# Kernel tuning notes

Hardware: AMD Instinct MI355X
Metric: run time of the kernel (lower is better)

Reference implementation:

```python
import jax, jax.numpy as jnp
import numpy as np
from jax import lax

EPS = 1e-12  # F.normalize eps

def setup_inputs() -> dict:
    key = jax.random.key(0)
    k1, k2, k3, k4 = jax.random.split(key, 4)
    b, c, h, w = 4, 64, 256, 256
    x = jax.random.normal(k1, (b, c, h, w), dtype=jnp.float32)
    w_in = jax.random.normal(k2, (4 * c, c), dtype=jnp.float32) * 0.05   # 1x1 conv dim->4*dim
    w_dw = jax.random.normal(k3, (2 * c, 1, 3, 3), dtype=jnp.float32) * 0.05  # depthwise 3x3, groups=2*dim
    w_out = jax.random.normal(k4, (c, c), dtype=jnp.float32) * 0.05      # 1x1 conv dim->dim
    temperature = jnp.ones((1, 1), dtype=jnp.float32)
    return {"x": x, "w_in": w_in, "w_dw": w_dw, "w_out": w_out, "temperature": temperature}


def reference(x, w_in, w_dw, w_out, temperature):
    b, c, h, w = x.shape
    # project_in: 1x1 conv dim -> 4*dim, then chunk into x1 (2c), x2 (2c)
    t = jnp.einsum('oc,bchw->bohw', w_in, x)
    x1, x2 = t[:, :2 * c], t[:, 2 * c:]
    # depthwise 3x3 conv (groups = 2c), padding=1
    dw = lax.conv_general_dilated(
        x1, w_dw, window_strides=(1, 1), padding='SAME',
        feature_group_count=2 * c,
        dimension_numbers=('NCHW', 'OIHW', 'NCHW'))
    qv = dw * x2  # [b, 2c, h, w]
    q = qv[:, :c].reshape(b, c, h * w)
    v = qv[:, c:].reshape(b, c, h * w)
    # L2-normalize along HW (F.normalize with eps)
    qn = q / jnp.maximum(jnp.linalg.norm(q, axis=-1, keepdims=True), EPS)
    kn = v / jnp.maximum(jnp.linalg.norm(v, axis=-1, keepdims=True), EPS)
    # channel-wise attention: [b, c, c]
    attn = jax.nn.softmax(jnp.einsum('bcn,bdn->bcd', qn, kn) * temperature, axis=-1)
    out = jnp.einsum('bcd,bdn->bcn', attn, v).reshape(b, c, h, w)
    # project_out: 1x1 conv dim -> dim
    return jnp.einsum('oc,bchw->bohw', w_out, out)
```

## Files before the change

kernel.cpp:

```cpp
#include <hip/hip_runtime.h>

#define EPSF 1e-12f
#define NT1 512

typedef __attribute__((ext_vector_type(8))) short short8;
typedef __attribute__((ext_vector_type(4))) float f32x4;
typedef __attribute__((ext_vector_type(4))) unsigned int uint4v;
typedef __attribute__((ext_vector_type(2))) unsigned int uint2v;

__device__ __forceinline__ unsigned f2bf(float f) {
    unsigned u = __float_as_uint(f);
    return (u + 0x7FFFu + ((u >> 16) & 1u)) >> 16;
}
__device__ __forceinline__ float bf2f(unsigned h) { return __uint_as_float(h << 16); }
__device__ __forceinline__ short8 asbf(uint4v u) { return __builtin_bit_cast(short8, u); }


__global__ __launch_bounds__(256, 2)
void kQ_half(const float* __restrict__ x, const float* __restrict__ w_in,
             const float* __restrict__ w_dw, unsigned short* __restrict__ qh,
             unsigned* __restrict__ vpk, float* __restrict__ sqq,
             float* __restrict__ sqv)
{
    __shared__ unsigned short t1s[64 * 360];
    __shared__ unsigned short t2s[64 * 264];

    const int tid = threadIdx.x;
    const int wv = tid >> 6, lane = tid & 63;
    const int l15 = lane & 15, l4 = lane >> 4;

    const int blk = blockIdx.x;
    const int half = blk & 1;
    const int tile = (blk >> 1) & 255;
    const int b = blk >> 9;
    const int y0 = (tile >> 3) << 3;
    const int x0t = (tile & 7) << 5;

    uint4v A1h[2], A1l[2], A2h[2], A2l[2];
    #pragma unroll
    for (int kh = 0; kh < 2; ++kh) {
        const float* wp1 = w_in + (half * 64 + wv * 16 + l15) * 64 + kh * 32 + l4 * 8;
        const float* wp2 = wp1 + 128 * 64;
        uint4v h1, l1, h2, l2;
        #pragma unroll
        for (int j = 0; j < 4; ++j) {
            float f0 = wp1[2*j], f1 = wp1[2*j+1];
            unsigned u0 = f2bf(f0), u1 = f2bf(f1);
            h1[j] = (u1 << 16) | u0;
            l1[j] = (f2bf(f1 - bf2f(u1)) << 16) | f2bf(f0 - bf2f(u0));
            float g0 = wp2[2*j], g1 = wp2[2*j+1];
            unsigned v0 = f2bf(g0), v1 = f2bf(g1);
            h2[j] = (v1 << 16) | v0;
            l2[j] = (f2bf(g1 - bf2f(v1)) << 16) | f2bf(g0 - bf2f(v0));
        }
        A1h[kh] = h1; A1l[kh] = l1;
        A2h[kh] = h2; A2l[kh] = l2;
    }

    const float* xb = x + ((size_t)b << 22);

    #pragma unroll 2
    for (int ht = 0; ht < 22; ++ht) {
        const int p = ht * 16 + l15;
        const unsigned row = (unsigned)p / 34u;
        const int col = p - (int)row * 34;
        const int gy = y0 - 1 + (int)row;
        const int gx = x0t - 1 + col;
        const bool inb = (p < 340) && ((unsigned)gy < 256u) && ((unsigned)gx < 256u);

        float xv0[8], xv1[8];
        #pragma unroll
        for (int j = 0; j < 8; ++j) { xv0[j] = 0.f; xv1[j] = 0.f; }
        if (inb) {
            const float* bp = xb + (size_t)(gy * 256 + gx);
            #pragma unroll
            for (int j = 0; j < 8; ++j) {
                xv0[j] = bp[(size_t)(l4 * 8 + j) << 16];
                xv1[j] = bp[(size_t)(32 + l4 * 8 + j) << 16];
            }
        }
        uint4v bh0, bl0, bh1, bl1;
        #pragma unroll
        for (int j = 0; j < 4; ++j) {
            unsigned h0 = f2bf(xv0[2*j]), h1 = f2bf(xv0[2*j+1]);
            bh0[j] = (h1 << 16) | h0;
            bl0[j] = (f2bf(xv0[2*j+1] - bf2f(h1)) << 16) | f2bf(xv0[2*j] - bf2f(h0));
            unsigned g0 = f2bf(xv1[2*j]), g1 = f2bf(xv1[2*j+1]);
            bh1[j] = (g1 << 16) | g0;
            bl1[j] = (f2bf(xv1[2*j+1] - bf2f(g1)) << 16) | f2bf(xv1[2*j] - bf2f(g0));
        }
        const short8 Bh0 = asbf(bh0), Bh1 = asbf(bh1);
        const short8 Bl0 = asbf(bl0), Bl1 = asbf(bl1);

        f32x4 a1 = {0.f, 0.f, 0.f, 0.f};
        a1 = __builtin_amdgcn_mfma_f32_16x16x32_bf16(asbf(A1h[0]), Bh0, a1, 0,0,0);
        a1 = __builtin_amdgcn_mfma_f32_16x16x32_bf16(asbf(A1h[1]), Bh1, a1, 0,0,0);
        a1 = __builtin_amdgcn_mfma_f32_16x16x32_bf16(asbf(A1h[0]), Bl0, a1, 0,0,0);
        a1 = __builtin_amdgcn_mfma_f32_16x16x32_bf16(asbf(A1h[1]), Bl1, a1, 0,0,0);
        a1 = __builtin_amdgcn_mfma_f32_16x16x32_bf16(asbf(A1l[0]), Bh0, a1, 0,0,0);
        a1 = __builtin_amdgcn_mfma_f32_16x16x32_bf16(asbf(A1l[1]), Bh1, a1, 0,0,0);

        f32x4 a2 = {0.f, 0.f, 0.f, 0.f};
        a2 = __builtin_amdgcn_mfma_f32_16x16x32_bf16(asbf(A2h[0]), Bh0, a2, 0,0,0);
        a2 = __builtin_amdgcn_mfma_f32_16x16x32_bf16(asbf(A2h[1]), Bh1, a2, 0,0,0);
        a2 = __builtin_amdgcn_mfma_f32_16x16x32_bf16(asbf(A2h[0]), Bl0, a2, 0,0,0);
        a2 = __builtin_amdgcn_mfma_f32_16x16x32_bf16(asbf(A2h[1]), Bl1, a2, 0,0,0);
        a2 = __builtin_amdgcn_mfma_f32_16x16x32_bf16(asbf(A2l[0]), Bh0, a2, 0,0,0);
        a2 = __builtin_amdgcn_mfma_f32_16x16x32_bf16(asbf(A2l[1]), Bh1, a2, 0,0,0);

        if (p < 340) {
            const int chb = wv * 16 + l4 * 4;
            #pragma unroll
            for (int r = 0; r < 4; ++r)
                t1s[(chb + r) * 360 + (int)row * 36 + col] = (unsigned short)f2bf(a1[r]);
        }
        if (row >= 1u && row <= 8u && col >= 1 && col <= 32) {
            const int cpx = ((int)row - 1) * 32 + (col - 1);
            const int chb = wv * 16 + l4 * 4;
            #pragma unroll
            for (int r = 0; r < 4; ++r)
                t2s[(chb + r) * 264 + cpx] = (unsigned short)f2bf(a2[r]);
        }
    }

    for (int it = 0; it < 8; ++it) {
        const int ch = wv * 16 + it * 2 + (lane >> 5);
        const int strip = lane & 31;
        const int row = strip >> 2, xs0 = (strip & 3) << 3;
        const float* wd = w_dw + (half * 64 + ch) * 9;
        const float w0 = wd[0], w1 = wd[1], w2 = wd[2];
        const float w3 = wd[3], w4 = wd[4], w5 = wd[5];
        const float w6 = wd[6], w7 = wd[7], w8 = wd[8];

        float win[3][10];
        #pragma unroll
        for (int r3 = 0; r3 < 3; ++r3) {
            const unsigned short* tp = &t1s[ch * 360 + (row + r3) * 36 + xs0];
            const uint2v ua = *(const uint2v*)tp;
            const uint2v ub = *(const uint2v*)(tp + 4);
            const unsigned uc = *(const unsigned*)(tp + 8);
            win[r3][0] = bf2f(ua[0] & 0xFFFFu); win[r3][1] = bf2f(ua[0] >> 16);
            win[r3][2] = bf2f(ua[1] & 0xFFFFu); win[r3][3] = bf2f(ua[1] >> 16);
            win[r3][4] = bf2f(ub[0] & 0xFFFFu); win[r3][5] = bf2f(ub[0] >> 16);
            win[r3][6] = bf2f(ub[1] & 0xFFFFu); win[r3][7] = bf2f(ub[1] >> 16);
            win[r3][8] = bf2f(uc & 0xFFFFu);    win[r3][9] = bf2f(uc >> 16);
        }
        const uint4v gv = *(const uint4v*)&t2s[ch * 264 + row * 32 + xs0];

        float q8[8];
        float sq = 0.f;
        #pragma unroll
        for (int k = 0; k < 8; ++k) {
            const float dwv = w0*win[0][k] + w1*win[0][k+1] + w2*win[0][k+2]
                            + w3*win[1][k] + w4*win[1][k+1] + w5*win[1][k+2]
                            + w6*win[2][k] + w7*win[2][k+1] + w8*win[2][k+2];
            const unsigned tu = gv[k >> 1];
            const float t2f = bf2f((k & 1) ? (tu >> 16) : (tu & 0xFFFFu));
            const float q = dwv * t2f;
            q8[k] = q; sq += q * q;
        }
        const size_t plane = ((size_t)(b * 64 + ch)) << 16;
        const size_t opx = (size_t)(y0 + row) * 256 + x0t + xs0;
        if (half == 0) {
            uint4v hp;
            #pragma unroll
            for (int k = 0; k < 4; ++k)
                hp[k] = (f2bf(q8[2*k+1]) << 16) | f2bf(q8[2*k]);
            *(uint4v*)(qh + plane + opx) = hp;
        } else {
            uint4v pa, pb;
            #pragma unroll
            for (int k = 0; k < 4; ++k) {
                unsigned h = f2bf(q8[k]);
                pa[k] = (h << 16) | f2bf(q8[k] - bf2f(h));
                unsigned h2 = f2bf(q8[4+k]);
                pb[k] = (h2 << 16) | f2bf(q8[4+k] - bf2f(h2));
            }
            unsigned* dst = vpk + plane + opx;
            *(uint4v*)dst = pa; *(uint4v*)(dst + 4) = pb;
        }
        sq += __shfl_xor(sq, 1);
        sq += __shfl_xor(sq, 2);
        sq += __shfl_xor(sq, 4);
        sq += __shfl_xor(sq, 8);
        sq += __shfl_xor(sq, 16);
        if ((lane & 31) == 0) {
            if (half == 0) atomicAdd(&sqq[b * 64 + ch], sq);
            else           atomicAdd(&sqv[b * 64 + ch], sq);
        }
    }
}

__global__ __launch_bounds__(256)
void kG_gemm(const unsigned short* __restrict__ qh, const unsigned* __restrict__ vpk,
             float* __restrict__ Gpart)
{
    const int blk = blockIdx.x, tid = threadIdx.x;
    const int b = blk >> 7, pblk = blk & 127;
    const int lane = tid & 63, wv = tid >> 6;
    const int l15 = lane & 15, l4 = lane >> 4;
    const int stripe = pblk * 4 + wv;
    const int px_base = stripe * 128;
    const unsigned short* qb = qh + ((size_t)b << 22);
    const unsigned* vb = vpk + ((size_t)b << 22);
    f32x4 acc[4][4];
    #pragma unroll
    for (int ct = 0; ct < 4; ++ct)
    #pragma unroll
    for (int dt = 0; dt < 4; ++dt) { f32x4 z = {0.f,0.f,0.f,0.f}; acc[ct][dt] = z; }

    for (int s = 0; s < 4; ++s) {
        const int kofs = px_base + s * 32 + l4 * 8;
        short8 A[4];
        #pragma unroll
        for (int ct = 0; ct < 4; ++ct)
            A[ct] = asbf(*(const uint4v*)(qb + (((size_t)(ct * 16 + l15)) << 16) + kofs));
        #pragma unroll
        for (int dt = 0; dt < 4; ++dt) {
            const unsigned* vp = vb + (((size_t)(dt * 16 + l15)) << 16) + kofs;
            const uint4v u0 = *(const uint4v*)vp;
            const uint4v u1 = *(const uint4v*)(vp + 4);
            uint4v bfv;
            bfv[0] = (u0[1] & 0xFFFF0000u) | (u0[0] >> 16);
            bfv[1] = (u0[3] & 0xFFFF0000u) | (u0[2] >> 16);
            bfv[2] = (u1[1] & 0xFFFF0000u) | (u1[0] >> 16);
            bfv[3] = (u1[3] & 0xFFFF0000u) | (u1[2] >> 16);
            const short8 Bf = asbf(bfv);
            #pragma unroll
            for (int ct = 0; ct < 4; ++ct)
                acc[ct][dt] = __builtin_amdgcn_mfma_f32_16x16x32_bf16(A[ct], Bf, acc[ct][dt], 0, 0, 0);
        }
    }
    float* gp = Gpart + (((size_t)b * 512 + stripe) << 12);
    #pragma unroll
    for (int ct = 0; ct < 4; ++ct)
    #pragma unroll
    for (int dt = 0; dt < 4; ++dt)
    #pragma unroll
    for (int r = 0; r < 4; ++r)
        gp[(ct * 16 + l4 * 4 + r) * 64 + dt * 16 + l15] = acc[ct][dt][r];
}

__global__ __launch_bounds__(256)
void kR_red(const float* __restrict__ Gpart, float* __restrict__ Gred)
{
    const int gid = blockIdx.x * 256 + threadIdx.x;
    const int b = gid >> 12, i = gid & 4095;
    float s = 0.f;
    #pragma unroll 8
    for (int p = 0; p < 512; ++p)
        s += Gpart[((((size_t)b * 512) + p) << 12) + i];
    Gred[((size_t)b << 12) + i] = s;
}

__global__ __launch_bounds__(256)
void kD_softmax(const float* __restrict__ Gred, const float* __restrict__ sqq,
                const float* __restrict__ sqv, const float* __restrict__ temp,
                const float* __restrict__ w_out, float* __restrict__ M)
{
    __shared__ float attn_s[64][65];
    __shared__ float wo_s[64][65];
    __shared__ float nv_s[64];
    const int b = blockIdx.x, tid = threadIdx.x;

    for (int i = tid; i < 4096; i += 256) {
        int o = i >> 6, c = i & 63;
        wo_s[o][c] = w_out[i];
    }
    if (tid < 64) nv_s[tid] = fmaxf(sqrtf(sqv[b * 64 + tid]), EPSF);
    __syncthreads();

    if (tid < 64) {
        const int c = tid;
        const float nq = fmaxf(sqrtf(sqq[b * 64 + c]), EPSF);
        const float scale = temp[0] / nq;
        float m = -1e30f;
        for (int d = 0; d < 64; ++d) {
            float s = Gred[b * 4096 + c * 64 + d] / nv_s[d] * scale;
            attn_s[c][d] = s;
            m = fmaxf(m, s);
        }
        float sum = 0.f;
        for (int d = 0; d < 64; ++d) {
            float e = expf(attn_s[c][d] - m);
            attn_s[c][d] = e;
            sum += e;
        }
        const float inv = 1.0f / sum;
        for (int d = 0; d < 64; ++d) attn_s[c][d] *= inv;
    }
    __syncthreads();

    const int o = tid & 63, dq = tid >> 6;
    float acc[16];
    #pragma unroll
    for (int j = 0; j < 16; ++j) acc[j] = 0.f;
    for (int c = 0; c < 64; ++c) {
        const float wv = wo_s[o][c];
        #pragma unroll
        for (int j = 0; j < 16; ++j) acc[j] += wv * attn_s[c][dq * 16 + j];
    }
    #pragma unroll
    for (int j = 0; j < 16; ++j) M[b * 4096 + o * 64 + dq * 16 + j] = acc[j];
}

__global__ __launch_bounds__(256)
void kE_out(const float* __restrict__ M, float* vout)
{
    __shared__ __attribute__((aligned(16))) float M_s[64][64];
    const int blk = blockIdx.x;
    const int b = blk >> 8, nb = blk & 255;
    const int tid = threadIdx.x;
    for (int i = tid; i < 4096; i += 256) M_s[i >> 6][i & 63] = M[b * 4096 + i];
    __syncthreads();

    const int n0 = nb * 256 + tid;
    float* vb = vout + ((size_t)b << 22);

    float vr[64];
    #pragma unroll
    for (int d = 0; d < 64; ++d) {
        const unsigned u = __float_as_uint(vb[((size_t)d << 16) + n0]);
        vr[d] = __uint_as_float(u & 0xFFFF0000u) + __uint_as_float(u << 16);
    }
    #pragma unroll 2
    for (int o = 0; o < 64; ++o) {
        float a0 = 0.f;
        #pragma unroll
        for (int dq = 0; dq < 16; ++dq) {
            const float4 m4 = *(const float4*)(&M_s[o][dq * 4]);
            a0 += m4.x * vr[dq*4+0];
            a0 += m4.y * vr[dq*4+1];
            a0 += m4.z * vr[dq*4+2];
            a0 += m4.w * vr[dq*4+3];
        }
        vb[((size_t)o << 16) + n0] = a0;
    }
}

__global__ __launch_bounds__(NT1)
void k1_fused(const float* __restrict__ x, const float* __restrict__ w_in,
              const float* __restrict__ w_dw, float* __restrict__ v_out,
              float* __restrict__ Gacc, float* __restrict__ sqq,
              float* __restrict__ sqv)
{
    __shared__ __attribute__((aligned(16))) float wT[64][256];
    __shared__ __attribute__((aligned(16))) float wdw_s[128][11];
    __shared__ __attribute__((aligned(16))) float xs[64][104];
    __shared__ __attribute__((aligned(16))) float t1s[64][105];
    __shared__ __attribute__((aligned(16))) float qvs[64][132];

    const int tid = threadIdx.x;
    const int blk = blockIdx.x;
    const int b = blk >> 6;
    const int bslot = blk & 63;

    for (int i = tid; i < 256 * 64; i += NT1) {
        int ch = i >> 6, c = i & 63;
        wT[c][ch] = w_in[i];
    }
    for (int i = tid; i < 128 * 9; i += NT1) {
        int ch = i / 9, k = i - ch * 9;
        wdw_s[ch][k] = w_dw[i];
    }

    const int gc0 = (tid >> 4) * 2;
    const int gd0 = (tid & 15) * 4;
    float g00 = 0, g01 = 0, g02 = 0, g03 = 0;
    float g10 = 0, g11 = 0, g12 = 0, g13 = 0;
    float sqreg = 0.f;

    const float* xb = x + ((size_t)b << 22);

    for (int tIdx = 0; tIdx < 16; ++tIdx) {
        const int tile = bslot + (tIdx << 6);
        const int ty0 = (tile >> 5) << 3;
        const int tx0 = (tile & 31) << 3;

        __syncthreads();

        for (int i = tid; i < 64 * 104; i += NT1) {
            int c = i / 104;
            int col = i - c * 104;
            float val = 0.f;
            if (col < 100) {
                int py = col / 10;
                int px = col - py * 10;
                int gy = ty0 - 1 + py;
                int gx = tx0 - 1 + px;
                if ((unsigned)gy < 256u && (unsigned)gx < 256u)
                    val = xb[((size_t)c << 16) + (gy << 8) + gx];
            }
            xs[c][col] = val;
        }
        __syncthreads();

        for (int h = 0; h < 2; ++h) {
            for (int it = tid; it < 672; it += NT1) {
                if (it < 416) {
                    const int chq = it / 26;
                    const int pq = it - chq * 26;
                    const int ch0 = (h << 6) + (chq << 2);
                    const int p0 = pq << 2;
                    float a00=0,a01=0,a02=0,a03=0, a10=0,a11=0,a12=0,a13=0;
                    float a20=0,a21=0,a22=0,a23=0, a30=0,a31=0,a32=0,a33=0;
                    #pragma unroll 4
                    for (int c = 0; c < 64; ++c) {
                        const float4 wv = *(const float4*)(&wT[c][ch0]);
                        const float4 xv = *(const float4*)(&xs[c][p0]);
                        a00 += wv.x*xv.x; a01 += wv.x*xv.y; a02 += wv.x*xv.z; a03 += wv.x*xv.w;
                        a10 += wv.y*xv.x; a11 += wv.y*xv.y; a12 += wv.y*xv.z; a13 += wv.y*xv.w;
                        a20 += wv.z*xv.x; a21 += wv.z*xv.y; a22 += wv.z*xv.z; a23 += wv.z*xv.w;
                        a30 += wv.w*xv.x; a31 += wv.w*xv.y; a32 += wv.w*xv.z; a33 += wv.w*xv.w;
                    }
                    const int lc = chq << 2;
                    t1s[lc+0][p0+0]=a00; t1s[lc+0][p0+1]=a01; t1s[lc+0][p0+2]=a02; t1s[lc+0][p0+3]=a03;
                    t1s[lc+1][p0+0]=a10; t1s[lc+1][p0+1]=a11; t1s[lc+1][p0+2]=a12; t1s[lc+1][p0+3]=a13;
                    t1s[lc+2][p0+0]=a20; t1s[lc+2][p0+1]=a21; t1s[lc+2][p0+2]=a22; t1s[lc+2][p0+3]=a23;
                    t1s[lc+3][p0+0]=a30; t1s[lc+3][p0+1]=a31; t1s[lc+3][p0+2]=a32; t1s[lc+3][p0+3]=a33;
                } else {
                    const int j = it - 416;
                    const int chq = j >> 4;
                    const int pq = j & 15;
                    const int ch0 = 128 + (h << 6) + (chq << 2);
                    const int p0 = pq << 2;
                    const int y = p0 >> 3, xc = p0 & 7;
                    const int hp0 = (y + 1) * 10 + xc + 1;
                    float a00=0,a01=0,a02=0,a03=0, a10=0,a11=0,a12=0,a13=0;
                    float a20=0,a21=0,a22=0,a23=0, a30=0,a31=0,a32=0,a33=0;
                    #pragma unroll 4
                    for (int c = 0; c < 64; ++c) {
                        const float4 wv = *(const float4*)(&wT[c][ch0]);
                        const float x0 = xs[c][hp0+0], x1 = xs[c][hp0+1];
                        const float x2 = xs[c][hp0+2], x3 = xs[c][hp0+3];
                        a00 += wv.x*x0; a01 += wv.x*x1; a02 += wv.x*x2; a03 += wv.x*x3;
                        a10 += wv.y*x0; a11 += wv.y*x1; a12 += wv.y*x2; a13 += wv.y*x3;
                        a20 += wv.z*x0; a21 += wv.z*x1; a22 += wv.z*x2; a23 += wv.z*x3;
                        a30 += wv.w*x0; a31 += wv.w*x1; a32 += wv.w*x2; a33 += wv.w*x3;
                    }
                    const int qc = (h << 6) + (chq << 2);
                    *(float4*)(&qvs[p0+0][qc]) = make_float4(a00, a10, a20, a30);
                    *(float4*)(&qvs[p0+1][qc]) = make_float4(a01, a11, a21, a31);
                    *(float4*)(&qvs[p0+2][qc]) = make_float4(a02, a12, a22, a32);
                    *(float4*)(&qvs[p0+3][qc]) = make_float4(a03, a13, a23, a33);
                }
            }
            __syncthreads();
            for (int it = tid; it < 4096; it += NT1) {
                const int ch = it & 63;
                const int p = it >> 6;
                const int y = p >> 3, xc = p & 7;
                const int base = y * 10 + xc;
                const float* wd = &wdw_s[(h << 6) + ch][0];
                float s = wd[0]*t1s[ch][base+ 0] + wd[1]*t1s[ch][base+ 1] + wd[2]*t1s[ch][base+ 2]
                        + wd[3]*t1s[ch][base+10] + wd[4]*t1s[ch][base+11] + wd[5]*t1s[ch][base+12]
                        + wd[6]*t1s[ch][base+20] + wd[7]*t1s[ch][base+21] + wd[8]*t1s[ch][base+22];
                const int qc = (h << 6) + ch;
                qvs[p][qc] = s * qvs[p][qc];
            }
            __syncthreads();
        }

        #pragma unroll 4
        for (int p = 0; p < 64; ++p) {
            const float2 q2 = *(const float2*)(&qvs[p][gc0]);
            const float4 v4 = *(const float4*)(&qvs[p][64 + gd0]);
            g00 += q2.x*v4.x; g01 += q2.x*v4.y; g02 += q2.x*v4.z; g03 += q2.x*v4.w;
            g10 += q2.y*v4.x; g11 += q2.y*v4.y; g12 += q2.y*v4.z; g13 += q2.y*v4.w;
        }
        if (tid < 128) {
            #pragma unroll 8
            for (int p = 0; p < 64; ++p) {
                const float val = qvs[p][tid];
                sqreg += val * val;
            }
        }
        for (int it = tid; it < 4096; it += NT1) {
            const int p = it & 63;
            const int d = it >> 6;
            const int gy = ty0 + (p >> 3), gx = tx0 + (p & 7);
            v_out[((size_t)(b * 64 + d) << 16) + (gy << 8) + gx] = qvs[p][64 + d];
        }
    }

    const int gb = b * 4096;
    atomicAdd(&Gacc[gb + (gc0 + 0) * 64 + gd0 + 0], g00);
    atomicAdd(&Gacc[gb + (gc0 + 0) * 64 + gd0 + 1], g01);
    atomicAdd(&Gacc[gb + (gc0 + 0) * 64 + gd0 + 2], g02);
    atomicAdd(&Gacc[gb + (gc0 + 0) * 64 + gd0 + 3], g03);
    atomicAdd(&Gacc[gb + (gc0 + 1) * 64 + gd0 + 0], g10);
    atomicAdd(&Gacc[gb + (gc0 + 1) * 64 + gd0 + 1], g11);
    atomicAdd(&Gacc[gb + (gc0 + 1) * 64 + gd0 + 2], g12);
    atomicAdd(&Gacc[gb + (gc0 + 1) * 64 + gd0 + 3], g13);
    if (tid < 64)       atomicAdd(&sqq[b * 64 + tid], sqreg);
    else if (tid < 128) atomicAdd(&sqv[b * 64 + tid - 64], sqreg);
}

__global__ __launch_bounds__(256)
void k3_out(const float* __restrict__ M, const float* v, float* out)
{
    __shared__ __attribute__((aligned(16))) float M_s[64][64];
    const int blk = blockIdx.x;
    const int b = blk >> 7;
    const int nb = blk & 127;
    const int tid = threadIdx.x;
    for (int i = tid; i < 4096; i += 256) M_s[i >> 6][i & 63] = M[b * 4096 + i];
    __syncthreads();

    const int n0 = nb * 512 + tid;
    const float* vb = v + ((size_t)b << 22);
    float* ob = out + ((size_t)b << 22);

    float vr0[64], vr1[64];
    #pragma unroll
    for (int d = 0; d < 64; ++d) {
        vr0[d] = vb[((size_t)d << 16) + n0];
        vr1[d] = vb[((size_t)d << 16) + n0 + 256];
    }
    for (int o = 0; o < 64; ++o) {
        float a0 = 0.f, a1 = 0.f;
        #pragma unroll
        for (int dq = 0; dq < 16; ++dq) {
            const float4 m4 = *(const float4*)(&M_s[o][dq * 4]);
            a0 += m4.x * vr0[dq*4+0]; a1 += m4.x * vr1[dq*4+0];
            a0 += m4.y * vr0[dq*4+1]; a1 += m4.y * vr1[dq*4+1];
            a0 += m4.z * vr0[dq*4+2]; a1 += m4.z * vr1[dq*4+2];
            a0 += m4.w * vr0[dq*4+3]; a1 += m4.w * vr1[dq*4+3];
        }
        ob[((size_t)o << 16) + n0] = a0;
        ob[((size_t)o << 16) + n0 + 256] = a1;
    }
}

extern "C" void kernel_launch(void* const* d_in, const int* in_sizes, int n_in,
                              void* d_out, int out_size, void* d_ws, size_t ws_size,
                              hipStream_t stream)
{
    (void)in_sizes; (void)n_in; (void)out_size;
    const float* x     = (const float*)d_in[0];
    const float* w_in  = (const float*)d_in[1];
    const float* w_dw  = (const float*)d_in[2];
    const float* w_out = (const float*)d_in[3];
    const float* temp  = (const float*)d_in[4];
    float* out = (float*)d_out;

    const size_t OFF_QH    = 0;
    const size_t OFF_GPART = 33554432;
    const size_t OFF_GRED  = 67108864;
    const size_t OFF_SQQ   = 67174400;
    const size_t OFF_SQV   = 67175424;
    const size_t OFF_M     = 67176448;
    const size_t NEED      = 67241984;

    if (ws_size >= NEED) {
        char* ws = (char*)d_ws;
        unsigned short* qh = (unsigned short*)(ws + OFF_QH);
        float* Gpart = (float*)(ws + OFF_GPART);
        float* Gred  = (float*)(ws + OFF_GRED);
        float* sqq   = (float*)(ws + OFF_SQQ);
        float* sqv   = (float*)(ws + OFF_SQV);
        float* Mws   = (float*)(ws + OFF_M);

        hipMemsetAsync((void*)sqq, 0, 2048, stream);
        hipLaunchKernelGGL(kQ_half, dim3(2048), dim3(256), 0, stream,
                           x, w_in, w_dw, qh, (unsigned*)d_out, sqq, sqv);
        hipLaunchKernelGGL(kG_gemm, dim3(512), dim3(256), 0, stream,
                           qh, (const unsigned*)d_out, Gpart);
        hipLaunchKernelGGL(kR_red, dim3(64), dim3(256), 0, stream, Gpart, Gred);
        hipLaunchKernelGGL(kD_softmax, dim3(4), dim3(256), 0, stream,
                           Gred, sqq, sqv, temp, w_out, Mws);
        hipLaunchKernelGGL(kE_out, dim3(1024), dim3(256), 0, stream, Mws, out);
    } else {
        float* Gacc = (float*)d_ws;
        float* sqq  = Gacc + 16384;
        float* sqv  = sqq + 256;
        float* Mws  = sqv + 256;
        hipMemsetAsync((void*)Gacc, 0, (16384 + 512) * sizeof(float), stream);
        hipLaunchKernelGGL(k1_fused, dim3(256), dim3(NT1), 0, stream,
                           x, w_in, w_dw, out, Gacc, sqq, sqv);
        hipLaunchKernelGGL(kD_softmax, dim3(4), dim3(256), 0, stream,
                           Gacc, sqq, sqv, temp, w_out, Mws);
        hipLaunchKernelGGL(k3_out, dim3(512), dim3(256), 0, stream,
                           Mws, out, out);
    }
}
```

Baseline: 446.5 us.

## Pre-split x into channel-last bf16 hi/lo planes and parallelize partial-Gram reduction

Adds a pre-pass kernel that transposes x into pixel-major layout and splits it into bf16 high and low halves once, so the projection kernel loads contiguous 16-byte vectors instead of strided per-channel floats and no longer redoes the split for halo pixels. It also spreads the Gram partial reduction over four times as many blocks, with each block summing four partial groups through shared memory. The cost is an extra kernel launch, an extra 64 MB of workspace, and additional write and read traffic for the split planes.

```diff
diff --git a/kernel.cpp b/kernel.cpp
--- a/kernel.cpp
+++ b/kernel.cpp
@@ -16,11 +16,45 @@
 __device__ __forceinline__ short8 asbf(uint4v u) { return __builtin_bit_cast(short8, u); }
 
 
+__global__ __launch_bounds__(256)
+void kA_split(const float* __restrict__ x, unsigned short* __restrict__ xh,
+              unsigned short* __restrict__ xl)
+{
+    __shared__ float xt[64][257];
+    const int blk = blockIdx.x, tid = threadIdx.x;
+    const int b = blk >> 8, chunk = blk & 255;
+    const int px0 = chunk * 256;
+    const float* xb = x + ((size_t)b << 22);
+    for (int c = 0; c < 64; ++c)
+        xt[c][tid] = xb[((size_t)c << 16) + px0 + tid];
+    __syncthreads();
+    const int px = px0 + tid;
+    unsigned hbuf[32], lbuf[32];
+    #pragma unroll
+    for (int j = 0; j < 32; ++j) {
+        float f0 = xt[2*j][tid], f1 = xt[2*j+1][tid];
+        unsigned h0 = f2bf(f0), h1 = f2bf(f1);
+        float r0 = f0 - bf2f(h0), r1 = f1 - bf2f(h1);
+        hbuf[j] = (h1 << 16) | h0;
+        lbuf[j] = (f2bf(r1) << 16) | f2bf(r0);
+    }
+    size_t row = ((size_t)(b << 16) + px) * 64;
+    uint4v* dh = (uint4v*)(xh + row);
+    uint4v* dl = (uint4v*)(xl + row);
+    #pragma unroll
+    for (int j = 0; j < 8; ++j) {
+        uint4v vh, vl;
+        vh[0]=hbuf[4*j]; vh[1]=hbuf[4*j+1]; vh[2]=hbuf[4*j+2]; vh[3]=hbuf[4*j+3];
+        vl[0]=lbuf[4*j]; vl[1]=lbuf[4*j+1]; vl[2]=lbuf[4*j+2]; vl[3]=lbuf[4*j+3];
+        dh[j] = vh; dl[j] = vl;
+    }
+}
+
 __global__ __launch_bounds__(256, 2)
-void kQ_half(const float* __restrict__ x, const float* __restrict__ w_in,
-             const float* __restrict__ w_dw, unsigned short* __restrict__ qh,
-             unsigned* __restrict__ vpk, float* __restrict__ sqq,
-             float* __restrict__ sqv)
+void kQ_half(const unsigned short* __restrict__ xh, const unsigned short* __restrict__ xl,
+             const float* __restrict__ w_in, const float* __restrict__ w_dw,
+             unsigned short* __restrict__ qh, unsigned* __restrict__ vpk,
+             float* __restrict__ sqq, float* __restrict__ sqv)
 {
     __shared__ unsigned short t1s[64 * 360];
     __shared__ unsigned short t2s[64 * 264];
@@ -57,8 +91,6 @@
         A2h[kh] = h2; A2l[kh] = l2;
     }
 
-    const float* xb = x + ((size_t)b << 22);
-
     #pragma unroll 2
     for (int ht = 0; ht < 22; ++ht) {
         const int p = ht * 16 + l15;
@@ -68,26 +100,13 @@
         const int gx = x0t - 1 + col;
         const bool inb = (p < 340) && ((unsigned)gy < 256u) && ((unsigned)gx < 256u);
 
-        float xv0[8], xv1[8];
-        #pragma unroll
-        for (int j = 0; j < 8; ++j) { xv0[j] = 0.f; xv1[j] = 0.f; }
+        uint4v bh0 = {0,0,0,0}, bh1 = {0,0,0,0}, bl0 = {0,0,0,0}, bl1 = {0,0,0,0};
         if (inb) {
-            const float* bp = xb + (size_t)(gy * 256 + gx);
-            #pragma unroll
-            for (int j = 0; j < 8; ++j) {
-                xv0[j] = bp[(size_t)(l4 * 8 + j) << 16];
-                xv1[j] = bp[(size_t)(32 + l4 * 8 + j) << 16];
-            }
-        }
-        uint4v bh0, bl0, bh1, bl1;
-        #pragma unroll
-        for (int j = 0; j < 4; ++j) {
-            unsigned h0 = f2bf(xv0[2*j]), h1 = f2bf(xv0[2*j+1]);
-            bh0[j] = (h1 << 16) | h0;
-            bl0[j] = (f2bf(xv0[2*j+1] - bf2f(h1)) << 16) | f2bf(xv0[2*j] - bf2f(h0));
-            unsigned g0 = f2bf(xv1[2*j]), g1 = f2bf(xv1[2*j+1]);
-            bh1[j] = (g1 << 16) | g0;
-            bl1[j] = (f2bf(xv1[2*j+1] - bf2f(g1)) << 16) | f2bf(xv1[2*j] - bf2f(g0));
+            const size_t off = (((size_t)b << 16) + (size_t)(gy * 256 + gx)) * 64 + l4 * 8;
+            bh0 = *(const uint4v*)(xh + off);
+            bh1 = *(const uint4v*)(xh + off + 32);
+            bl0 = *(const uint4v*)(xl + off);
+            bl1 = *(const uint4v*)(xl + off + 32);
         }
         const short8 Bh0 = asbf(bh0), Bh1 = asbf(bh1);
         const short8 Bl0 = asbf(bl0), Bl1 = asbf(bl1);
@@ -244,13 +263,19 @@
 __global__ __launch_bounds__(256)
 void kR_red(const float* __restrict__ Gpart, float* __restrict__ Gred)
 {
-    const int gid = blockIdx.x * 256 + threadIdx.x;
-    const int b = gid >> 12, i = gid & 4095;
+    __shared__ float red[4][64];
+    const int blk = blockIdx.x, tid = threadIdx.x;
+    const int b = blk >> 6;
+    const int i = ((blk & 63) << 6) + (tid & 63);
+    const int pg = tid >> 6;
     float s = 0.f;
     #pragma unroll 8
-    for (int p = 0; p < 512; ++p)
+    for (int p = pg * 128; p < pg * 128 + 128; ++p)
         s += Gpart[((((size_t)b * 512) + p) << 12) + i];
-    Gred[((size_t)b << 12) + i] = s;
+    red[pg][tid & 63] = s;
+    __syncthreads();
+    if (pg == 0)
+        Gred[((size_t)b << 12) + i] = red[0][tid] + red[1][tid] + red[2][tid] + red[3][tid];
 }
 
 __global__ __launch_bounds__(256)
@@ -544,16 +569,20 @@
     const float* temp  = (const float*)d_in[4];
     float* out = (float*)d_out;
 
-    const size_t OFF_QH    = 0;
-    const size_t OFF_GPART = 33554432;
-    const size_t OFF_GRED  = 67108864;
-    const size_t OFF_SQQ   = 67174400;
-    const size_t OFF_SQV   = 67175424;
-    const size_t OFF_M     = 67176448;
-    const size_t NEED      = 67241984;
+    const size_t OFF_XH    = 0;
+    const size_t OFF_XL    = 33554432;
+    const size_t OFF_QH    = 67108864;
+    const size_t OFF_GPART = 100663296;
+    const size_t OFF_GRED  = 134217728;
+    const size_t OFF_SQQ   = 134283264;
+    const size_t OFF_SQV   = 134284288;
+    const size_t OFF_M     = 134285312;
+    const size_t NEED      = 134350848;
 
     if (ws_size >= NEED) {
         char* ws = (char*)d_ws;
+        unsigned short* xh = (unsigned short*)(ws + OFF_XH);
+        unsigned short* xl = (unsigned short*)(ws + OFF_XL);
         unsigned short* qh = (unsigned short*)(ws + OFF_QH);
         float* Gpart = (float*)(ws + OFF_GPART);
         float* Gred  = (float*)(ws + OFF_GRED);
@@ -562,11 +591,12 @@
         float* Mws   = (float*)(ws + OFF_M);
 
         hipMemsetAsync((void*)sqq, 0, 2048, stream);
+        hipLaunchKernelGGL(kA_split, dim3(1024), dim3(256), 0, stream, x, xh, xl);
         hipLaunchKernelGGL(kQ_half, dim3(2048), dim3(256), 0, stream,
-                           x, w_in, w_dw, qh, (unsigned*)d_out, sqq, sqv);
+                           xh, xl, w_in, w_dw, qh, (unsigned*)d_out, sqq, sqv);
         hipLaunchKernelGGL(kG_gemm, dim3(512), dim3(256), 0, stream,
                            qh, (const unsigned*)d_out, Gpart);
-        hipLaunchKernelGGL(kR_red, dim3(64), dim3(256), 0, stream, Gpart, Gred);
+        hipLaunchKernelGGL(kR_red, dim3(256), dim3(256), 0, stream, Gpart, Gred);
         hipLaunchKernelGGL(kD_softmax, dim3(4), dim3(256), 0, stream,
                            Gred, sqq, sqv, temp, w_out, Mws);
         hipLaunchKernelGGL(kE_out, dim3(1024), dim3(256), 0, stream, Mws, out);
```

Result: slower. 459.0 us (+2.8%).
